# Kernel tuning notes

Measured on AMD Instinct MI355X. Metric: run time of the kernel, lower is better.

The kernel has to match this reference:

```python
import jax, jax.numpy as jnp
import numpy as np

# Static conv hyperparameters (match init_kwargs)
STRIDE = (1, 1)
PAD = (1, 1)
DIL = (1, 1)
GROUPS = 1
DG = 1  # num_deformable_groups


def setup_inputs() -> dict:
    key = jax.random.key(0)
    k1, k2, k3 = jax.random.split(key, 3)
    B, C, H, W = 4, 256, 64, 64
    OC, kh, kw = 256, 3, 3
    x = jax.random.normal(k1, (B, C, H, W), dtype=jnp.float32)
    # offset: [B, DG*2*kh*kw, Ho, Wo], ordered (tap, [dy, dx]) per deformable group
    offset = jax.random.normal(k2, (B, DG * 2 * kh * kw, H, W), dtype=jnp.float32)
    n = C * kh * kw
    stdv = 1.0 / np.sqrt(n)
    weight = jax.random.uniform(k3, (OC, C // GROUPS, kh, kw), dtype=jnp.float32,
                                minval=-stdv, maxval=stdv)
    return {"x": x, "offset": offset, "weight": weight}


def _deform_conv(x, offset, weight):
    B, C, H, W = x.shape
    OC, Cg_w, kh, kw = weight.shape
    sh, sw = STRIDE
    ph, pw = PAD
    dh, dw = DIL
    Ho = (H + 2 * ph - (dh * (kh - 1) + 1)) // sh + 1
    Wo = (W + 2 * pw - (dw * (kw - 1) + 1)) // sw + 1
    K = kh * kw
    Cg = C // DG  # channels per deformable group

    # offsets: [B, DG, K, 2, Ho, Wo]; channel 0 = dy (h), channel 1 = dx (w)
    off = offset.reshape(B, DG, K, 2, Ho, Wo)

    # base (undeformed) sampling positions per tap
    ki, kj = jnp.meshgrid(jnp.arange(kh), jnp.arange(kw), indexing='ij')
    base_h = (jnp.arange(Ho) * sh - ph)[None, :] + (ki.reshape(-1) * dh)[:, None]  # [K, Ho]
    base_w = (jnp.arange(Wo) * sw - pw)[None, :] + (kj.reshape(-1) * dw)[:, None]  # [K, Wo]

    pos_h = base_h[None, None, :, :, None].astype(x.dtype) + off[:, :, :, 0]  # [B,DG,K,Ho,Wo]
    pos_w = base_w[None, None, :, None, :].astype(x.dtype) + off[:, :, :, 1]  # [B,DG,K,Ho,Wo]

    h0f = jnp.floor(pos_h)
    w0f = jnp.floor(pos_w)
    lh = pos_h - h0f  # fractional parts
    lw = pos_w - w0f
    h0 = h0f.astype(jnp.int32)
    w0 = w0f.astype(jnp.int32)

    xg = x.reshape(B, DG, Cg, H * W)

    def gather(hi, wi):
        # zero-padded gather: out-of-range corners contribute 0 (mmcv DCNv1 semantics)
        valid = (hi >= 0) & (hi < H) & (wi >= 0) & (wi < W)  # [B,DG,K,Ho,Wo]
        idx = jnp.clip(hi, 0, H - 1) * W + jnp.clip(wi, 0, W - 1)
        flat = idx.reshape(B, DG, 1, K * Ho * Wo)
        vals = jnp.take_along_axis(
            xg, jnp.broadcast_to(flat, (B, DG, Cg, K * Ho * Wo)), axis=3)
        vals = vals.reshape(B, DG, Cg, K, Ho, Wo)
        return vals * valid[:, :, None].astype(x.dtype)

    # bilinear interpolation over 4 corners -> im2col columns [B,DG,Cg,K,Ho,Wo]
    cols = (gather(h0, w0) * ((1 - lh) * (1 - lw))[:, :, None]
            + gather(h0, w0 + 1) * ((1 - lh) * lw)[:, :, None]
            + gather(h0 + 1, w0) * (lh * (1 - lw))[:, :, None]
            + gather(h0 + 1, w0 + 1) * (lh * lw)[:, :, None])

    # grouped GEMM: columns x weight
    cols = cols.reshape(B, GROUPS, C // GROUPS, K, Ho, Wo)
    wg = weight.reshape(GROUPS, OC // GROUPS, Cg_w, K)
    out = jnp.einsum('gock,bgckhw->bgohw', wg, cols)
    return out.reshape(B, OC, Ho, Wo)


def reference(x, offset, weight):
    return _deform_conv(x, offset, weight)
```

## Files before the change

### kernel.cpp

```cpp
#include <hip/hip_runtime.h>
#include <hip/hip_bf16.h>
#include <math.h>


constexpr int B  = 4;
constexpr int C  = 256;
constexpr int H  = 64;
constexpr int W  = 64;
constexpr int OC = 256;
constexpr int Ho = 64;
constexpr int Wo = 64;

constexpr int NT     = 64;
constexpr int CHUNKS = 72;
constexpr int KCH    = 36;
constexpr int WROW   = 40;

constexpr size_t WB_ELTS  = (size_t)CHUNKS * 16 * 512;
constexpr size_t XB_ELTS  = (size_t)B * 8 * 4096 * 32;
constexpr size_t OUT_ELTS = (size_t)B * OC * Ho * Wo;

typedef __attribute__((ext_vector_type(8))) short bf16x8;
typedef __attribute__((ext_vector_type(4))) float f32x4;

__device__ __forceinline__ float bf_lo(unsigned u) {
    union { unsigned i; float f; } c; c.i = u << 16; return c.f;
}
__device__ __forceinline__ float bf_hi(unsigned u) {
    union { unsigned i; float f; } c; c.i = u & 0xffff0000u; return c.f;
}
__device__ __forceinline__ ushort fbf(float f) {
    __hip_bfloat16 h = __float2bfloat16(f); return *(ushort*)&h;
}

__global__ __launch_bounds__(256)
void prep_all(const float* __restrict__ x, const float* __restrict__ wt,
              ushort* __restrict__ xb, ushort* __restrict__ wB)
{
    __shared__ ushort sx[128 * WROW];
    __shared__ ushort sw[CHUNKS * WROW];
    const int t = threadIdx.x;

    if (blockIdx.x < 1024) {
        const int blk = blockIdx.x;
        const int hwb = blk & 31;
        const int cb  = (blk >> 5) & 7;
        const int b   = blk >> 8;
        const int hw0 = hwb << 7;
        const int lhw = t & 127, chalf = t >> 7;
        #pragma unroll
        for (int i = 0; i < 16; ++i) {
            const int c = i * 2 + chalf;
            sx[lhw * WROW + c] =
                fbf(x[(((size_t)(b * 256 + cb * 32 + c)) << 12) + hw0 + lhw]);
        }
        __syncthreads();
        const int whw = t >> 1, wh = t & 1;
        const uint4 v0 = *(const uint4*)&sx[whw * WROW + wh * 16];
        const uint4 v1 = *(const uint4*)&sx[whw * WROW + wh * 16 + 8];
        uint4* dst = (uint4*)(xb + ((size_t)((b * 8 + cb) * 4096 + hw0) << 5));
        dst[whw * 4 + wh * 2 + 0] = v0;
        dst[whw * 4 + wh * 2 + 1] = v1;
    } else {
        const int oc = blockIdx.x - 1024;
        const int c  = t, chb = c >> 5, kk = c & 31;
        const float* wp = wt + ((size_t)oc * C + c) * 9;
        #pragma unroll
        for (int tap = 0; tap < 9; ++tap)
            sw[(tap * 8 + chb) * WROW + kk] = fbf(wp[tap]);
        __syncthreads();
        const int og = oc >> 4, mr = oc & 15;
        for (int i = t; i < CHUNKS * 4; i += 256) {
            const int ch = i >> 2, kq = i & 3;
            *(uint4*)(wB + ((size_t)ch * 16 + og) * 512 + (kq * 16 + mr) * 8) =
                *(const uint4*)&sw[ch * WROW + kq * 8];
        }
    }
}

struct GathRegs { uint4 c00, c01, c10, c11; float4 mw; };

__global__ __launch_bounds__(512, 4)
void dcn_mfma(const ushort* __restrict__ xb, const float* __restrict__ off,
              const ushort* __restrict__ wB, float* __restrict__ po)
{
    __shared__ __align__(16) ushort s_col[2][2][NT * WROW];

    const int xcd = blockIdx.x & 7;
    const int ii  = blockIdx.x >> 3;
    const int b   = xcd & 3;
    const int khalf = ii & 1;
    const int ho  = ((xcd >> 2) << 5) + (ii >> 1);
    const int ch0 = khalf * KCH;
    float* outp = po + (size_t)khalf * OUT_ELTS;
    const int tid = threadIdx.x;

    const int lane = tid & 63;
    const int wv   = tid >> 6;
    const int kq   = lane >> 4;
    const int mr   = lane & 15;

    const int kc_t = tid >> 8;
    const int st   = tid & 255;
    const int sn   = st >> 2;
    const int sgg  = st & 3;
    const ushort* xb_sg = xb + ((size_t)b << 20) + (sgg << 3);

    f32x4 acc[2][4];
    #pragma unroll
    for (int mt = 0; mt < 2; ++mt)
        #pragma unroll
        for (int nt = 0; nt < 4; ++nt)
            acc[mt][nt] = (f32x4){0.f, 0.f, 0.f, 0.f};

    int   ctap = -1;
    int2  mi   = make_int2(0, 0);
    float4 mwv = make_float4(0.f, 0.f, 0.f, 0.f);
    auto upd_meta = [&](int p) {
        const int ch  = ch0 + 2 * p + kc_t;
        const int tap = ch >> 3;
        if (tap != ctap) {
            ctap = tap;
            const float dy = off[((size_t)(b * 18 + 2 * tap)     * Ho + ho) * Wo + sn];
            const float dx = off[((size_t)(b * 18 + 2 * tap + 1) * Ho + ho) * Wo + sn];
            const float ph = (float)(ho - 1 + tap / 3) + dy;
            const float pw = (float)(sn - 1 + tap % 3) + dx;
            const float h0f = floorf(ph), w0f = floorf(pw);
            const int h0 = (int)h0f, w0 = (int)w0f;
            const float lh = ph - h0f, lw = pw - w0f;
            const int wb = min(max(w0, 0), W - 2);
            const int ht = min(max(h0, 0), H - 1);
            const int hb = min(max(h0 + 1, 0), H - 1);
            const float s0 = (wb == w0) ? (1.f - lw) : ((wb == w0 + 1) ? lw : 0.f);
            const float s1 = (wb + 1 == w0 + 1) ? lw : ((wb + 1 == w0) ? (1.f - lw) : 0.f);
            const float wtp = (h0 >= 0 && h0 < H)         ? (1.f - lh) : 0.f;
            const float wbt = (h0 + 1 >= 0 && h0 + 1 < H) ? lh         : 0.f;
            mi  = make_int2(ht * W + wb, hb * W + wb);
            mwv = make_float4(wtp * s0, wtp * s1, wbt * s0, wbt * s1);
        }
    };

    auto issueg = [&](int p, GathRegs& g) {
        const int ch  = ch0 + 2 * p + kc_t;
        const int cb  = ch & 7;
        g.mw = mwv;
        const ushort* xp = xb_sg + ((size_t)cb << 17);
        g.c00 = *(const uint4*)(xp + ((size_t)mi.x << 5));
        g.c01 = *(const uint4*)(xp + (((size_t)mi.x + 1) << 5));
        g.c10 = *(const uint4*)(xp + ((size_t)mi.y << 5));
        g.c11 = *(const uint4*)(xp + (((size_t)mi.y + 1) << 5));
    };
    auto sampfma = [&](const GathRegs& g, int buf) {
        union { ushort pk[8]; uint4 v; } u;
        const unsigned a00[4] = {g.c00.x, g.c00.y, g.c00.z, g.c00.w};
        const unsigned a01[4] = {g.c01.x, g.c01.y, g.c01.z, g.c01.w};
        const unsigned a10[4] = {g.c10.x, g.c10.y, g.c10.z, g.c10.w};
        const unsigned a11[4] = {g.c11.x, g.c11.y, g.c11.z, g.c11.w};
        #pragma unroll
        for (int j = 0; j < 4; ++j) {
            const float vlo = g.mw.x * bf_lo(a00[j]) + g.mw.y * bf_lo(a01[j])
                            + g.mw.z * bf_lo(a10[j]) + g.mw.w * bf_lo(a11[j]);
            const float vhi = g.mw.x * bf_hi(a00[j]) + g.mw.y * bf_hi(a01[j])
                            + g.mw.z * bf_hi(a10[j]) + g.mw.w * bf_hi(a11[j]);
            u.pk[2 * j]     = fbf(vlo);
            u.pk[2 * j + 1] = fbf(vhi);
        }
        *(uint4*)&s_col[buf][kc_t][sn * WROW + sgg * 8] = u.v;
    };
    auto phase = [&](int p, const GathRegs& gcur, int buf) {
        bf16x8 wf[2][2];
        const int chb = ch0 + 2 * p;
        #pragma unroll
        for (int kc = 0; kc < 2; ++kc)
            #pragma unroll
            for (int mt = 0; mt < 2; ++mt)
                wf[kc][mt] = *(const bf16x8*)
                    (wB + ((size_t)(chb + kc) * 16 + wv * 2 + mt) * 512 + lane * 8);
        sampfma(gcur, buf);
        asm volatile("s_waitcnt lgkmcnt(0)" ::: "memory");
        __builtin_amdgcn_s_barrier();
        __builtin_amdgcn_sched_barrier(0);
        __builtin_amdgcn_s_setprio(1);
        #pragma unroll
        for (int kc = 0; kc < 2; ++kc)
            #pragma unroll
            for (int nt = 0; nt < 4; ++nt) {
                const bf16x8 bfr = *(const bf16x8*)
                    &s_col[buf][kc][(nt * 16 + mr) * WROW + kq * 8];
                #pragma unroll
                for (int mt = 0; mt < 2; ++mt)
                    acc[mt][nt] = __builtin_amdgcn_mfma_f32_16x16x32_bf16(
                        wf[kc][mt], bfr, acc[mt][nt], 0, 0, 0);
            }
        __builtin_amdgcn_s_setprio(0);
    };

    GathRegs gA, gB;
    upd_meta(0);
    issueg(0, gA);

    #pragma unroll 1
    for (int it = 0; it < 9; ++it) {
        upd_meta(2 * it + 1);
        issueg(2 * it + 1, gB);
        phase(2 * it, gA, 0);
        if (it < 8) {
            upd_meta(2 * it + 2);
            issueg(2 * it + 2, gA);
        }
        phase(2 * it + 1, gB, 1);
    }

    #pragma unroll
    for (int mt = 0; mt < 2; ++mt)
        #pragma unroll
        for (int nt = 0; nt < 4; ++nt)
            #pragma unroll
            for (int r = 0; r < 4; ++r) {
                const int oc = wv * 32 + mt * 16 + kq * 4 + r;
                const int wo = nt * 16 + mr;
                outp[((size_t)(b * OC + oc) * Ho + ho) * Wo + wo] = acc[mt][nt][r];
            }
}

__global__ __launch_bounds__(256)
void reduce2(const float4* __restrict__ p0, const float4* __restrict__ p1,
             float4* __restrict__ out)
{
    const int i = blockIdx.x * 256 + threadIdx.x;
    const float4 a = p0[i], b = p1[i];
    out[i] = make_float4(a.x + b.x, a.y + b.y, a.z + b.z, a.w + b.w);
}

extern "C" void kernel_launch(void* const* d_in, const int* in_sizes, int n_in,
                              void* d_out, int out_size, void* d_ws, size_t ws_size,
                              hipStream_t stream)
{
    const float* x   = (const float*)d_in[0];
    const float* off = (const float*)d_in[1];
    const float* wt  = (const float*)d_in[2];
    float* out = (float*)d_out;

    ushort* wB = (ushort*)d_ws;
    ushort* xb = wB + WB_ELTS;
    float*  po = (float*)(xb + XB_ELTS);

    prep_all<<<1280, 256, 0, stream>>>(x, wt, xb, wB);
    dcn_mfma<<<512, 512, 0, stream>>>(xb, off, wB, po);
    reduce2<<<(int)(OUT_ELTS / 4 / 256), 256, 0, stream>>>(
        (const float4*)po, (const float4*)(po + OUT_ELTS), (float4*)out);
}
```

Measured before the change: 123.0 us.

## Replace split-K across blocks with intra-block split-K and LDS reduction

Instead of splitting the 72 K-chunks across two blocks that write partial outputs to global memory and then running a separate reduce kernel, each block now covers all chunks. Its 8 waves split into 4 output-channel groups times 2 K halves, and the two halves' accumulators are combined through LDS before the final store. This removes the partial-output round trip through global memory and one kernel launch. It also prefetches the next tap's offsets ahead of use. In exchange the grid halves to 256 blocks, each wave holds twice the accumulators, and launch bounds drop to 2 blocks per CU, so occupancy and latency hiding may suffer.

```diff
diff --git a/kernel.cpp b/kernel.cpp
--- a/kernel.cpp
+++ b/kernel.cpp
@@ -13,12 +13,10 @@
 
 constexpr int NT     = 64;
 constexpr int CHUNKS = 72;
-constexpr int KCH    = 36;
 constexpr int WROW   = 40;
 
 constexpr size_t WB_ELTS  = (size_t)CHUNKS * 16 * 512;
 constexpr size_t XB_ELTS  = (size_t)B * 8 * 4096 * 32;
-constexpr size_t OUT_ELTS = (size_t)B * OC * Ho * Wo;
 
 typedef __attribute__((ext_vector_type(8))) short bf16x8;
 typedef __attribute__((ext_vector_type(4))) float f32x4;
@@ -80,23 +78,21 @@
 
 struct GathRegs { uint4 c00, c01, c10, c11; float4 mw; };
 
-__global__ __launch_bounds__(512, 4)
+__global__ __launch_bounds__(512, 2)
 void dcn_mfma(const ushort* __restrict__ xb, const float* __restrict__ off,
-              const ushort* __restrict__ wB, float* __restrict__ po)
+              const ushort* __restrict__ wB, float* __restrict__ out)
 {
     __shared__ __align__(16) ushort s_col[2][2][NT * WROW];
 
     const int xcd = blockIdx.x & 7;
-    const int ii  = blockIdx.x >> 3;
     const int b   = xcd & 3;
-    const int khalf = ii & 1;
-    const int ho  = ((xcd >> 2) << 5) + (ii >> 1);
-    const int ch0 = khalf * KCH;
-    float* outp = po + (size_t)khalf * OUT_ELTS;
+    const int ho  = ((xcd >> 2) << 5) + (blockIdx.x >> 3);
     const int tid = threadIdx.x;
 
     const int lane = tid & 63;
     const int wv   = tid >> 6;
+    const int ocg  = wv & 3;
+    const int kside= wv >> 2;
     const int kq   = lane >> 4;
     const int mr   = lane & 15;
 
@@ -106,43 +102,46 @@
     const int sgg  = st & 3;
     const ushort* xb_sg = xb + ((size_t)b << 20) + (sgg << 3);
 
-    f32x4 acc[2][4];
+    f32x4 acc[4][4];
     #pragma unroll
-    for (int mt = 0; mt < 2; ++mt)
+    for (int mt = 0; mt < 4; ++mt)
         #pragma unroll
         for (int nt = 0; nt < 4; ++nt)
             acc[mt][nt] = (f32x4){0.f, 0.f, 0.f, 0.f};
 
-    int   ctap = -1;
-    int2  mi   = make_int2(0, 0);
-    float4 mwv = make_float4(0.f, 0.f, 0.f, 0.f);
-    auto upd_meta = [&](int p) {
-        const int ch  = ch0 + 2 * p + kc_t;
+    int    ctap = 0;
+    int2   mi;
+    float4 mwv;
+    float  pdy = 0.f, pdx = 0.f;
+    auto compute_meta = [&](int tap, float dy, float dx) {
+        const float ph = (float)(ho - 1 + tap / 3) + dy;
+        const float pw = (float)(sn - 1 + tap % 3) + dx;
+        const float h0f = floorf(ph), w0f = floorf(pw);
+        const int h0 = (int)h0f, w0 = (int)w0f;
+        const float lh = ph - h0f, lw = pw - w0f;
+        const int wb = min(max(w0, 0), W - 2);
+        const int ht = min(max(h0, 0), H - 1);
+        const int hb = min(max(h0 + 1, 0), H - 1);
+        const float s0 = (wb == w0) ? (1.f - lw) : ((wb == w0 + 1) ? lw : 0.f);
+        const float s1 = (wb + 1 == w0 + 1) ? lw : ((wb + 1 == w0) ? (1.f - lw) : 0.f);
+        const float wtp = (h0 >= 0 && h0 < H)         ? (1.f - lh) : 0.f;
+        const float wbt = (h0 + 1 >= 0 && h0 + 1 < H) ? lh         : 0.f;
+        mi  = make_int2(ht * W + wb, hb * W + wb);
+        mwv = make_float4(wtp * s0, wtp * s1, wbt * s0, wbt * s1);
+    };
+    auto load_off = [&](int tap, float& dy, float& dx) {
+        dy = off[((size_t)(b * 18 + 2 * tap)     * Ho + ho) * Wo + sn];
+        dx = off[((size_t)(b * 18 + 2 * tap + 1) * Ho + ho) * Wo + sn];
+    };
+    auto pre = [&](int p) {
+        const int ch  = 2 * p + kc_t;
         const int tap = ch >> 3;
-        if (tap != ctap) {
-            ctap = tap;
-            const float dy = off[((size_t)(b * 18 + 2 * tap)     * Ho + ho) * Wo + sn];
-            const float dx = off[((size_t)(b * 18 + 2 * tap + 1) * Ho + ho) * Wo + sn];
-            const float ph = (float)(ho - 1 + tap / 3) + dy;
-            const float pw = (float)(sn - 1 + tap % 3) + dx;
-            const float h0f = floorf(ph), w0f = floorf(pw);
-            const int h0 = (int)h0f, w0 = (int)w0f;
-            const float lh = ph - h0f, lw = pw - w0f;
-            const int wb = min(max(w0, 0), W - 2);
-            const int ht = min(max(h0, 0), H - 1);
-            const int hb = min(max(h0 + 1, 0), H - 1);
-            const float s0 = (wb == w0) ? (1.f - lw) : ((wb == w0 + 1) ? lw : 0.f);
-            const float s1 = (wb + 1 == w0 + 1) ? lw : ((wb + 1 == w0) ? (1.f - lw) : 0.f);
-            const float wtp = (h0 >= 0 && h0 < H)         ? (1.f - lh) : 0.f;
-            const float wbt = (h0 + 1 >= 0 && h0 + 1 < H) ? lh         : 0.f;
-            mi  = make_int2(ht * W + wb, hb * W + wb);
-            mwv = make_float4(wtp * s0, wtp * s1, wbt * s0, wbt * s1);
-        }
+        if (tap != ctap) { compute_meta(tap, pdy, pdx); ctap = tap; }
+        if ((ch & 6) == 4 && tap < 8) load_off(tap + 1, pdy, pdx);
     };
 
     auto issueg = [&](int p, GathRegs& g) {
-        const int ch  = ch0 + 2 * p + kc_t;
-        const int cb  = ch & 7;
+        const int cb = (2 * p + kc_t) & 7;
         g.mw = mwv;
         const ushort* xp = xb_sg + ((size_t)cb << 17);
         g.c00 = *(const uint4*)(xp + ((size_t)mi.x << 5));
@@ -168,68 +167,75 @@
         *(uint4*)&s_col[buf][kc_t][sn * WROW + sgg * 8] = u.v;
     };
     auto phase = [&](int p, const GathRegs& gcur, int buf) {
-        bf16x8 wf[2][2];
-        const int chb = ch0 + 2 * p;
-        #pragma unroll
-        for (int kc = 0; kc < 2; ++kc)
-            #pragma unroll
-            for (int mt = 0; mt < 2; ++mt)
-                wf[kc][mt] = *(const bf16x8*)
-                    (wB + ((size_t)(chb + kc) * 16 + wv * 2 + mt) * 512 + lane * 8);
+        bf16x8 wf[4];
+        const int ch = 2 * p + kside;
+        #pragma unroll
+        for (int mt = 0; mt < 4; ++mt)
+            wf[mt] = *(const bf16x8*)
+                (wB + ((size_t)ch * 16 + ocg * 4 + mt) * 512 + lane * 8);
         sampfma(gcur, buf);
         asm volatile("s_waitcnt lgkmcnt(0)" ::: "memory");
         __builtin_amdgcn_s_barrier();
         __builtin_amdgcn_sched_barrier(0);
         __builtin_amdgcn_s_setprio(1);
         #pragma unroll
-        for (int kc = 0; kc < 2; ++kc)
+        for (int nt = 0; nt < 4; ++nt) {
+            const bf16x8 bfr = *(const bf16x8*)
+                &s_col[buf][kside][(nt * 16 + mr) * WROW + kq * 8];
+            #pragma unroll
+            for (int mt = 0; mt < 4; ++mt)
+                acc[mt][nt] = __builtin_amdgcn_mfma_f32_16x16x32_bf16(
+                    wf[mt], bfr, acc[mt][nt], 0, 0, 0);
+        }
+        __builtin_amdgcn_s_setprio(0);
+    };
+
+    {
+        float dy0, dx0;
+        load_off(0, dy0, dx0);
+        compute_meta(0, dy0, dx0);
+    }
+    GathRegs gA, gB;
+    issueg(0, gA);
+
+    #pragma unroll 1
+    for (int it = 0; it < 18; ++it) {
+        pre(2 * it + 1);
+        issueg(2 * it + 1, gB);
+        phase(2 * it, gA, 0);
+        if (it < 17) {
+            pre(2 * it + 2);
+            issueg(2 * it + 2, gA);
+        }
+        phase(2 * it + 1, gB, 1);
+    }
+
+    float4* red = (float4*)s_col;
+    #pragma unroll 1
+    for (int mt = 0; mt < 4; ++mt) {
+        __syncthreads();
+        if (kside == 1) {
+            #pragma unroll
+            for (int nt = 0; nt < 4; ++nt)
+                red[(ocg * 4 + nt) * 64 + lane] =
+                    make_float4(acc[mt][nt][0], acc[mt][nt][1],
+                                acc[mt][nt][2], acc[mt][nt][3]);
+        }
+        __syncthreads();
+        if (kside == 0) {
             #pragma unroll
             for (int nt = 0; nt < 4; ++nt) {
-                const bf16x8 bfr = *(const bf16x8*)
-                    &s_col[buf][kc][(nt * 16 + mr) * WROW + kq * 8];
+                const float4 o = red[(ocg * 4 + nt) * 64 + lane];
                 #pragma unroll
-                for (int mt = 0; mt < 2; ++mt)
-                    acc[mt][nt] = __builtin_amdgcn_mfma_f32_16x16x32_bf16(
-                        wf[kc][mt], bfr, acc[mt][nt], 0, 0, 0);
+                for (int r = 0; r < 4; ++r) {
+                    const int oc = ocg * 64 + mt * 16 + kq * 4 + r;
+                    const int wo = nt * 16 + mr;
+                    out[((size_t)(b * OC + oc) * Ho + ho) * Wo + wo] =
+                        acc[mt][nt][r] + ((const float*)&o)[r];
+                }
             }
-        __builtin_amdgcn_s_setprio(0);
-    };
-
-    GathRegs gA, gB;
-    upd_meta(0);
-    issueg(0, gA);
-
-    #pragma unroll 1
-    for (int it = 0; it < 9; ++it) {
-        upd_meta(2 * it + 1);
-        issueg(2 * it + 1, gB);
-        phase(2 * it, gA, 0);
-        if (it < 8) {
-            upd_meta(2 * it + 2);
-            issueg(2 * it + 2, gA);
-        }
-        phase(2 * it + 1, gB, 1);
-    }
-
-    #pragma unroll
-    for (int mt = 0; mt < 2; ++mt)
-        #pragma unroll
-        for (int nt = 0; nt < 4; ++nt)
-            #pragma unroll
-            for (int r = 0; r < 4; ++r) {
-                const int oc = wv * 32 + mt * 16 + kq * 4 + r;
-                const int wo = nt * 16 + mr;
-                outp[((size_t)(b * OC + oc) * Ho + ho) * Wo + wo] = acc[mt][nt][r];
-            }
-}
-
-__global__ __launch_bounds__(256)
-void reduce2(const float4* __restrict__ p0, const float4* __restrict__ p1,
-             float4* __restrict__ out)
-{
-    const int i = blockIdx.x * 256 + threadIdx.x;
-    const float4 a = p0[i], b = p1[i];
-    out[i] = make_float4(a.x + b.x, a.y + b.y, a.z + b.z, a.w + b.w);
+        }
+    }
 }
 
 extern "C" void kernel_launch(void* const* d_in, const int* in_sizes, int n_in,
@@ -243,10 +249,7 @@
 
     ushort* wB = (ushort*)d_ws;
     ushort* xb = wB + WB_ELTS;
-    float*  po = (float*)(xb + XB_ELTS);
 
     prep_all<<<1280, 256, 0, stream>>>(x, wt, xb, wB);
-    dcn_mfma<<<512, 512, 0, stream>>>(xb, off, wB, po);
-    reduce2<<<(int)(OUT_ELTS / 4 / 256), 256, 0, stream>>>(
-        (const float4*)po, (const float4*)(po + OUT_ELTS), (float4*)out);
-}
+    dcn_mfma<<<256, 512, 0, stream>>>(xb, off, wB, out);
+}
```

After: 124.7 us. Within noise of the previous version (+1.4%).

## Split work by output-width half instead of K-half, drop partial-sum reduce

Applied to the files above, without the earlier changes.

Each block now covers 32 output columns over the full 72-chunk K range instead of 64 columns over half of K. This removes the fp32 partial-output buffers and the separate reduce kernel. Per-tap sampling metadata is precomputed once into shared memory by the first 288 threads rather than recomputed per thread. Results are staged through LDS so global stores are coalesced float4 writes. In exchange, each block issues twice as many weight-fragment loads per output element and runs fewer MFMA N-tiles per phase.

```diff
diff --git a/kernel.cpp b/kernel.cpp
--- a/kernel.cpp
+++ b/kernel.cpp
@@ -11,14 +11,12 @@
 constexpr int Ho = 64;
 constexpr int Wo = 64;
 
-constexpr int NT     = 64;
+constexpr int NPOS   = 32;
 constexpr int CHUNKS = 72;
-constexpr int KCH    = 36;
-constexpr int WROW   = 40;
+constexpr int WROW   = 34;
 
 constexpr size_t WB_ELTS  = (size_t)CHUNKS * 16 * 512;
 constexpr size_t XB_ELTS  = (size_t)B * 8 * 4096 * 32;
-constexpr size_t OUT_ELTS = (size_t)B * OC * Ho * Wo;
 
 typedef __attribute__((ext_vector_type(8))) short bf16x8;
 typedef __attribute__((ext_vector_type(4))) float f32x4;
@@ -33,12 +31,13 @@
     __hip_bfloat16 h = __float2bfloat16(f); return *(ushort*)&h;
 }
 
+constexpr int XROW = 40;
 __global__ __launch_bounds__(256)
 void prep_all(const float* __restrict__ x, const float* __restrict__ wt,
               ushort* __restrict__ xb, ushort* __restrict__ wB)
 {
-    __shared__ ushort sx[128 * WROW];
-    __shared__ ushort sw[CHUNKS * WROW];
+    __shared__ ushort sx[128 * XROW];
+    __shared__ ushort sw[CHUNKS * XROW];
     const int t = threadIdx.x;
 
     if (blockIdx.x < 1024) {
@@ -51,13 +50,13 @@
         #pragma unroll
         for (int i = 0; i < 16; ++i) {
             const int c = i * 2 + chalf;
-            sx[lhw * WROW + c] =
+            sx[lhw * XROW + c] =
                 fbf(x[(((size_t)(b * 256 + cb * 32 + c)) << 12) + hw0 + lhw]);
         }
         __syncthreads();
         const int whw = t >> 1, wh = t & 1;
-        const uint4 v0 = *(const uint4*)&sx[whw * WROW + wh * 16];
-        const uint4 v1 = *(const uint4*)&sx[whw * WROW + wh * 16 + 8];
+        const uint4 v0 = *(const uint4*)&sx[whw * XROW + wh * 16];
+        const uint4 v1 = *(const uint4*)&sx[whw * XROW + wh * 16 + 8];
         uint4* dst = (uint4*)(xb + ((size_t)((b * 8 + cb) * 4096 + hw0) << 5));
         dst[whw * 4 + wh * 2 + 0] = v0;
         dst[whw * 4 + wh * 2 + 1] = v1;
@@ -67,13 +66,13 @@
         const float* wp = wt + ((size_t)oc * C + c) * 9;
         #pragma unroll
         for (int tap = 0; tap < 9; ++tap)
-            sw[(tap * 8 + chb) * WROW + kk] = fbf(wp[tap]);
+            sw[(tap * 8 + chb) * XROW + kk] = fbf(wp[tap]);
         __syncthreads();
         const int og = oc >> 4, mr = oc & 15;
         for (int i = t; i < CHUNKS * 4; i += 256) {
             const int ch = i >> 2, kq = i & 3;
             *(uint4*)(wB + ((size_t)ch * 16 + og) * 512 + (kq * 16 + mr) * 8) =
-                *(const uint4*)&sw[ch * WROW + kq * 8];
+                *(const uint4*)&sw[ch * XROW + kq * 8];
         }
     }
 }
@@ -82,67 +81,73 @@
 
 __global__ __launch_bounds__(512, 4)
 void dcn_mfma(const ushort* __restrict__ xb, const float* __restrict__ off,
-              const ushort* __restrict__ wB, float* __restrict__ po)
+              const ushort* __restrict__ wB, float* __restrict__ out)
 {
-    __shared__ __align__(16) ushort s_col[2][2][NT * WROW];
-
-    const int xcd = blockIdx.x & 7;
-    const int ii  = blockIdx.x >> 3;
-    const int b   = xcd & 3;
-    const int khalf = ii & 1;
-    const int ho  = ((xcd >> 2) << 5) + (ii >> 1);
-    const int ch0 = khalf * KCH;
-    float* outp = po + (size_t)khalf * OUT_ELTS;
-    const int tid = threadIdx.x;
+    __shared__ __align__(16) ushort s_mem[16384];
+    ushort (*s_col)[4][NPOS * WROW] = (ushort (*)[4][NPOS * WROW])s_mem;
+    int2*   s_midx = (int2*)  (s_mem + 8704);
+    float4* s_mw   = (float4*)(s_mem + 9856);
+
+    const int xcd    = blockIdx.x & 7;
+    const int inner  = blockIdx.x >> 3;
+    const int b      = xcd & 3;
+    const int wohalf = inner & 1;
+    const int ho     = ((xcd >> 2) << 5) + (inner >> 1);
+    const int wo0    = wohalf << 5;
+    const int tid    = threadIdx.x;
+
+    if (tid < 9 * NPOS) {
+        const int tap = tid >> 5, sn = tid & 31;
+        const float dy = off[((size_t)(b * 18 + 2 * tap)     * Ho + ho) * Wo + wo0 + sn];
+        const float dx = off[((size_t)(b * 18 + 2 * tap + 1) * Ho + ho) * Wo + wo0 + sn];
+        const float ph = (float)(ho - 1 + tap / 3) + dy;
+        const float pw = (float)(wo0 + sn - 1 + tap % 3) + dx;
+        const float h0f = floorf(ph), w0f = floorf(pw);
+        const int h0 = (int)h0f, w0 = (int)w0f;
+        const float lh = ph - h0f, lw = pw - w0f;
+        const int wb = min(max(w0, 0), W - 2);
+        const int ht = min(max(h0, 0), H - 1);
+        const int hb = min(max(h0 + 1, 0), H - 1);
+        const float s0 = (wb == w0) ? (1.f - lw) : ((wb == w0 + 1) ? lw : 0.f);
+        const float s1 = (wb + 1 == w0 + 1) ? lw : ((wb + 1 == w0) ? (1.f - lw) : 0.f);
+        const float wtp = (h0 >= 0 && h0 < H)         ? (1.f - lh) : 0.f;
+        const float wbt = (h0 + 1 >= 0 && h0 + 1 < H) ? lh         : 0.f;
+        s_midx[tid] = make_int2(ht * W + wb, hb * W + wb);
+        s_mw[tid]   = make_float4(wtp * s0, wtp * s1, wbt * s0, wbt * s1);
+    }
 
     const int lane = tid & 63;
     const int wv   = tid >> 6;
     const int kq   = lane >> 4;
     const int mr   = lane & 15;
 
-    const int kc_t = tid >> 8;
-    const int st   = tid & 255;
+    const int kc_t = tid >> 7;
+    const int st   = tid & 127;
     const int sn   = st >> 2;
     const int sgg  = st & 3;
     const ushort* xb_sg = xb + ((size_t)b << 20) + (sgg << 3);
 
-    f32x4 acc[2][4];
+    f32x4 acc[2][2];
     #pragma unroll
     for (int mt = 0; mt < 2; ++mt)
         #pragma unroll
-        for (int nt = 0; nt < 4; ++nt)
+        for (int nt = 0; nt < 2; ++nt)
             acc[mt][nt] = (f32x4){0.f, 0.f, 0.f, 0.f};
 
-    int   ctap = -1;
-    int2  mi   = make_int2(0, 0);
-    float4 mwv = make_float4(0.f, 0.f, 0.f, 0.f);
-    auto upd_meta = [&](int p) {
-        const int ch  = ch0 + 2 * p + kc_t;
-        const int tap = ch >> 3;
+    int    ctap = -1;
+    int2   mi;
+    float4 mwv;
+    auto refresh = [&](int p) {
+        const int tap = (4 * p + kc_t) >> 3;
         if (tap != ctap) {
             ctap = tap;
-            const float dy = off[((size_t)(b * 18 + 2 * tap)     * Ho + ho) * Wo + sn];
-            const float dx = off[((size_t)(b * 18 + 2 * tap + 1) * Ho + ho) * Wo + sn];
-            const float ph = (float)(ho - 1 + tap / 3) + dy;
-            const float pw = (float)(sn - 1 + tap % 3) + dx;
-            const float h0f = floorf(ph), w0f = floorf(pw);
-            const int h0 = (int)h0f, w0 = (int)w0f;
-            const float lh = ph - h0f, lw = pw - w0f;
-            const int wb = min(max(w0, 0), W - 2);
-            const int ht = min(max(h0, 0), H - 1);
-            const int hb = min(max(h0 + 1, 0), H - 1);
-            const float s0 = (wb == w0) ? (1.f - lw) : ((wb == w0 + 1) ? lw : 0.f);
-            const float s1 = (wb + 1 == w0 + 1) ? lw : ((wb + 1 == w0) ? (1.f - lw) : 0.f);
-            const float wtp = (h0 >= 0 && h0 < H)         ? (1.f - lh) : 0.f;
-            const float wbt = (h0 + 1 >= 0 && h0 + 1 < H) ? lh         : 0.f;
-            mi  = make_int2(ht * W + wb, hb * W + wb);
-            mwv = make_float4(wtp * s0, wtp * s1, wbt * s0, wbt * s1);
+            mi  = s_midx[tap * NPOS + sn];
+            mwv = s_mw  [tap * NPOS + sn];
         }
     };
 
     auto issueg = [&](int p, GathRegs& g) {
-        const int ch  = ch0 + 2 * p + kc_t;
-        const int cb  = ch & 7;
+        const int cb = (4 * p + kc_t) & 7;
         g.mw = mwv;
         const ushort* xp = xb_sg + ((size_t)cb << 17);
         g.c00 = *(const uint4*)(xp + ((size_t)mi.x << 5));
@@ -168,23 +173,22 @@
         *(uint4*)&s_col[buf][kc_t][sn * WROW + sgg * 8] = u.v;
     };
     auto phase = [&](int p, const GathRegs& gcur, int buf) {
-        bf16x8 wf[2][2];
-        const int chb = ch0 + 2 * p;
-        #pragma unroll
-        for (int kc = 0; kc < 2; ++kc)
+        bf16x8 wf[4][2];
+        #pragma unroll
+        for (int kc = 0; kc < 4; ++kc)
             #pragma unroll
             for (int mt = 0; mt < 2; ++mt)
                 wf[kc][mt] = *(const bf16x8*)
-                    (wB + ((size_t)(chb + kc) * 16 + wv * 2 + mt) * 512 + lane * 8);
+                    (wB + ((size_t)(4 * p + kc) * 16 + wv * 2 + mt) * 512 + lane * 8);
         sampfma(gcur, buf);
         asm volatile("s_waitcnt lgkmcnt(0)" ::: "memory");
         __builtin_amdgcn_s_barrier();
         __builtin_amdgcn_sched_barrier(0);
         __builtin_amdgcn_s_setprio(1);
         #pragma unroll
-        for (int kc = 0; kc < 2; ++kc)
+        for (int kc = 0; kc < 4; ++kc)
             #pragma unroll
-            for (int nt = 0; nt < 4; ++nt) {
+            for (int nt = 0; nt < 2; ++nt) {
                 const bf16x8 bfr = *(const bf16x8*)
                     &s_col[buf][kc][(nt * 16 + mr) * WROW + kq * 8];
                 #pragma unroll
@@ -195,41 +199,41 @@
         __builtin_amdgcn_s_setprio(0);
     };
 
+    __syncthreads();
+
     GathRegs gA, gB;
-    upd_meta(0);
+    refresh(0);
     issueg(0, gA);
 
     #pragma unroll 1
     for (int it = 0; it < 9; ++it) {
-        upd_meta(2 * it + 1);
+        refresh(2 * it + 1);
         issueg(2 * it + 1, gB);
         phase(2 * it, gA, 0);
         if (it < 8) {
-            upd_meta(2 * it + 2);
+            refresh(2 * it + 2);
             issueg(2 * it + 2, gA);
         }
         phase(2 * it + 1, gB, 1);
     }
 
+    __syncthreads();
+    float* mysf = (float*)s_mem + wv * 1024;
     #pragma unroll
     for (int mt = 0; mt < 2; ++mt)
         #pragma unroll
-        for (int nt = 0; nt < 4; ++nt)
+        for (int nt = 0; nt < 2; ++nt)
             #pragma unroll
-            for (int r = 0; r < 4; ++r) {
-                const int oc = wv * 32 + mt * 16 + kq * 4 + r;
-                const int wo = nt * 16 + mr;
-                outp[((size_t)(b * OC + oc) * Ho + ho) * Wo + wo] = acc[mt][nt][r];
-            }
-}
-
-__global__ __launch_bounds__(256)
-void reduce2(const float4* __restrict__ p0, const float4* __restrict__ p1,
-             float4* __restrict__ out)
-{
-    const int i = blockIdx.x * 256 + threadIdx.x;
-    const float4 a = p0[i], b = p1[i];
-    out[i] = make_float4(a.x + b.x, a.y + b.y, a.z + b.z, a.w + b.w);
+            for (int r = 0; r < 4; ++r)
+                mysf[(mt * 16 + kq * 4 + r) * 32 + nt * 16 + mr] = acc[mt][nt][r];
+    #pragma unroll
+    for (int j = 0; j < 4; ++j) {
+        const int idx = j * 64 + lane;
+        const int row = idx >> 3, q = idx & 7;
+        const float4 v = *(const float4*)&mysf[row * 32 + q * 4];
+        const int oc = wv * 32 + row;
+        *(float4*)&out[(((size_t)(b * OC + oc) * Ho + ho) << 6) + wo0 + q * 4] = v;
+    }
 }
 
 extern "C" void kernel_launch(void* const* d_in, const int* in_sizes, int n_in,
@@ -243,10 +247,7 @@
 
     ushort* wB = (ushort*)d_ws;
     ushort* xb = wB + WB_ELTS;
-    float*  po = (float*)(xb + XB_ELTS);
 
     prep_all<<<1280, 256, 0, stream>>>(x, wt, xb, wB);
-    dcn_mfma<<<512, 512, 0, stream>>>(xb, off, wB, po);
-    reduce2<<<(int)(OUT_ELTS / 4 / 256), 256, 0, stream>>>(
-        (const float4*)po, (const float4*)(po + OUT_ELTS), (float4*)out);
-}
+    dcn_mfma<<<512, 512, 0, stream>>>(xb, off, wB, out);
+}
```

Result: slower. 153.2 us (+24.6%).
